# Optimization experiments

Hardware: AMD Instinct MI355X
Metric: run time of the kernel (lower is better)

The kernel has to match this reference:

```python
import jax, jax.numpy as jnp
import numpy as np

D_MODEL = 512
N_HEAD = 8
D_K = 64
EPS = 1e-5


def setup_inputs() -> dict:
    key = jax.random.key(0)
    ks = jax.random.split(key, 12)
    B, S = 4, 2048
    Q = jax.random.normal(ks[0], (B, S, D_MODEL), dtype=jnp.float32)
    K = jax.random.normal(ks[1], (B, S, D_MODEL), dtype=jnp.float32)
    V = jax.random.normal(ks[2], (B, S, D_MODEL), dtype=jnp.float32)
    # bool padding-style mask: True = masked position
    att_mask = jax.random.randint(ks[3], (B, S, S), 0, 2).astype(bool)
    s = 1.0 / np.sqrt(D_MODEL)
    # Linear weights stored as [in, out] (transpose of torch's [out, in]; same math)
    Wq = jax.random.uniform(ks[4], (D_MODEL, N_HEAD * D_K), jnp.float32, -s, s)
    bq = jax.random.uniform(ks[5], (N_HEAD * D_K,), jnp.float32, -s, s)
    Wk = jax.random.uniform(ks[6], (D_MODEL, N_HEAD * D_K), jnp.float32, -s, s)
    bk = jax.random.uniform(ks[7], (N_HEAD * D_K,), jnp.float32, -s, s)
    Wv = jax.random.uniform(ks[8], (D_MODEL, N_HEAD * D_K), jnp.float32, -s, s)
    bv = jax.random.uniform(ks[9], (N_HEAD * D_K,), jnp.float32, -s, s)
    Wo = jax.random.uniform(ks[10], (N_HEAD * D_K, D_MODEL), jnp.float32, -s, s)
    bo = jax.random.uniform(ks[11], (D_MODEL,), jnp.float32, -s, s)
    return {"Q": Q, "K": K, "V": V, "att_mask": att_mask,
            "Wq": Wq, "bq": bq, "Wk": Wk, "bk": bk,
            "Wv": Wv, "bv": bv, "Wo": Wo, "bo": bo}


def _layer_norm(x):
    # nn.LayerNorm with default weight=1, bias=0 (fresh module in forward)
    mu = jnp.mean(x, axis=-1, keepdims=True)
    var = jnp.mean(jnp.square(x - mu), axis=-1, keepdims=True)
    return (x - mu) / jnp.sqrt(var + EPS)


def reference(Q, K, V, att_mask, Wq, bq, Wk, bk, Wv, bv, Wo, bo):
    B, S, _ = Q.shape
    residual = Q
    # QKV projections -> [B, H, S, Dk]
    q = (Q @ Wq + bq).reshape(B, S, N_HEAD, D_K).transpose(0, 2, 1, 3)
    k = (K @ Wk + bk).reshape(B, S, N_HEAD, D_K).transpose(0, 2, 1, 3)
    v = (V @ Wv + bv).reshape(B, S, N_HEAD, D_K).transpose(0, 2, 1, 3)
    # scaled dot-product attention with padding mask
    score = jnp.einsum('bhqd,bhkd->bhqk', q, k) / np.sqrt(D_K)
    score = jnp.where(att_mask[:, None, :, :], jnp.float32(-1e9), score)
    attn = jax.nn.softmax(score, axis=-1)
    context = jnp.einsum('bhqk,bhkd->bhqd', attn, v)
    context = context.transpose(0, 2, 1, 3).reshape(B, S, N_HEAD * D_K)
    output = context @ Wo + bo
    out = _layer_norm(output + residual)
    return out, attn
```

## Files before the change

### kernel.cpp

```cpp
#include <hip/hip_runtime.h>
#include <hip/hip_bf16.h>
#include <cstdint>
#include <cstddef>


typedef __attribute__((ext_vector_type(8)))  short short8v;
typedef __attribute__((ext_vector_type(2)))  float f32x2;
typedef __attribute__((ext_vector_type(4)))  float f32x4;
typedef __attribute__((ext_vector_type(16))) float f32x16;

constexpr int DM = 512, S = 2048, BATCH = 4, NHEAD = 8, DK = 64;
constexpr int ROWS = BATCH * S;
constexpr int BH   = BATCH * NHEAD;
constexpr size_t OUT_ELEMS = (size_t)ROWS * DM;
constexpr size_t HFRAG = 131072;

#define ZERO16 {0.f,0.f,0.f,0.f,0.f,0.f,0.f,0.f,0.f,0.f,0.f,0.f,0.f,0.f,0.f,0.f}

__device__ __forceinline__ unsigned short f2bf(float f) {
    union { __hip_bfloat16 b; unsigned short u; } c;
    c.b = __float2bfloat16(f);
    return c.u;
}
__device__ __forceinline__ float bf2f(unsigned short u) {
    union { float f; unsigned u32; } c;
    c.u32 = (unsigned)u << 16;
    return c.f;
}

__global__ __launch_bounds__(256)
void wconv(const float* __restrict__ Wq, const float* __restrict__ Wk,
           const float* __restrict__ Wv, const float* __restrict__ Wo,
           unsigned short* __restrict__ wt)
{
    __shared__ float T[32][33];
    const float* srcs[4] = {Wq, Wk, Wv, Wo};
    const float* W = srcs[blockIdx.z];
    unsigned short* out = wt + (size_t)blockIdx.z * DM * DM;
    const int r0 = blockIdx.y * 32, c0 = blockIdx.x * 32;
    const int tid = threadIdx.x;
#pragma unroll
    for (int i = 0; i < 4; ++i) {
        int lin = tid + i * 256; int r = lin >> 5, c = lin & 31;
        T[r][c] = W[(size_t)(r0 + r) * DM + c0 + c];
    }
    __syncthreads();
#pragma unroll
    for (int i = 0; i < 4; ++i) {
        int lin = tid + i * 256; int rn = lin >> 5, ck = lin & 31;
        out[(size_t)(c0 + rn) * DM + r0 + ck] = f2bf(T[ck][rn]);
    }
}

__global__ __launch_bounds__(256)
void maskpack(const uint8_t* __restrict__ mask, unsigned* __restrict__ mb)
{
    const int t = threadIdx.x;
    const int row = blockIdx.x * 4 + (t >> 6);
    const int w = t & 63;
    const uint8_t* src = mask + (size_t)row * S + 32 * w;
    const uint4 a = *reinterpret_cast<const uint4*>(src);
    const uint4 b = *reinterpret_cast<const uint4*>(src + 16);
    const unsigned m8[8] = {a.x, a.y, a.z, a.w, b.x, b.y, b.z, b.w};
    unsigned bits = 0;
#pragma unroll
    for (int k2 = 0; k2 < 32; ++k2)
        bits |= (((m8[k2 >> 2] >> (8 * (k2 & 3))) & 0xffu) ? 1u : 0u) << k2;
    mb[(size_t)row * 64 + w] = bits;
}

__global__ __launch_bounds__(256)
void proj3_mfma(const float* __restrict__ Qin, const float* __restrict__ Kin,
                const float* __restrict__ Vin, const unsigned short* __restrict__ wt,
                const float* __restrict__ bq, const float* __restrict__ bk,
                const float* __restrict__ bv,
                unsigned short* __restrict__ qo, unsigned short* __restrict__ ko,
                unsigned short* __restrict__ vo)
{
    const int z = blockIdx.z;
    const float* X = (z == 0) ? Qin : (z == 1) ? Kin : Vin;
    const unsigned short* Wt = wt + (size_t)z * DM * DM;
    const float* bias = (z == 0) ? bq : (z == 1) ? bk : bv;
    unsigned short* Y = (z == 0) ? qo : (z == 1) ? ko : vo;
    const float scale = (z == 0) ? 0.125f : 1.0f;

    const int tid = threadIdx.x, wv = tid >> 6, l = tid & 63, lr = l & 31, lh = l >> 5;
    const int m0 = blockIdx.y * 128 + wv * 32;
    const int n0 = blockIdx.x * 64;
    const float* xp = X + (size_t)(m0 + lr) * DM + 8 * lh;
    const unsigned short* w0 = Wt + (size_t)(n0 + lr) * DM + 8 * lh;
    const unsigned short* w1 = w0 + (size_t)32 * DM;
    f32x16 acc0 = ZERO16, acc1 = ZERO16;
#pragma unroll 8
    for (int t = 0; t < 32; ++t) {
        float4 xa = *reinterpret_cast<const float4*>(xp + 16 * t);
        float4 xb = *reinterpret_cast<const float4*>(xp + 16 * t + 4);
        short8v a;
        a[0] = (short)f2bf(xa.x * scale); a[1] = (short)f2bf(xa.y * scale);
        a[2] = (short)f2bf(xa.z * scale); a[3] = (short)f2bf(xa.w * scale);
        a[4] = (short)f2bf(xb.x * scale); a[5] = (short)f2bf(xb.y * scale);
        a[6] = (short)f2bf(xb.z * scale); a[7] = (short)f2bf(xb.w * scale);
        short8v b0 = *reinterpret_cast<const short8v*>(w0 + 16 * t);
        short8v b1 = *reinterpret_cast<const short8v*>(w1 + 16 * t);
        acc0 = __builtin_amdgcn_mfma_f32_32x32x16_bf16(a, b0, acc0, 0, 0, 0);
        acc1 = __builtin_amdgcn_mfma_f32_32x32x16_bf16(a, b1, acc1, 0, 0, 0);
    }
#pragma unroll
    for (int j = 0; j < 2; ++j) {
        const f32x16 acc = j ? acc1 : acc0;
        const int n = n0 + 32 * j + lr;
        const float bvv = bias[n] * scale;
        const int h = n >> 6, d = n & 63;
#pragma unroll
        for (int r = 0; r < 16; ++r) {
            const int m = m0 + (r & 3) + 8 * (r >> 2) + 4 * lh;
            const int bb = m >> 11, s = m & (S - 1);
            const int bh = bb * NHEAD + h;
            const unsigned short val = f2bf(acc[r] + bvv);
            size_t idx;
            if (z == 0)
                idx = ((size_t)bh * S + s) * DK + d;
            else if (z == 1)
                idx = (size_t)bh * HFRAG + (size_t)(s >> 4) * 1024 + (size_t)(d >> 5) * 512
                      + (size_t)(((s & 15) + 16 * ((d & 31) >> 3)) << 3) + (d & 7);
            else
                idx = (size_t)bh * HFRAG + (size_t)(s >> 5) * 2048 + (size_t)(d >> 4) * 512
                      + (size_t)(((d & 15) + 16 * ((s & 31) >> 3)) << 3) + (s & 7);
            Y[idx] = val;
        }
    }
}

__global__ __launch_bounds__(512, 4)
void attn_fused(const unsigned short* __restrict__ q,
                const unsigned short* __restrict__ kpack,
                const unsigned short* __restrict__ vpack,
                const unsigned* __restrict__ mbits,
                float* __restrict__ attn,
                unsigned short* __restrict__ ctx)
{
    __shared__ char Pc[16 * 4096];
    __shared__ float cred[2][4][16][16];
    __shared__ float redm[8][16];
    __shared__ float reds[8][16];
    const int tid = threadIdx.x, wv = tid >> 6, l = tid & 63;
    const int lq = l & 15, lg = l >> 4;
    const int bid = blockIdx.x;
    const int bh = 4 * (bid & 7) + ((bid >> 3) & 3);
    const int q0 = (bid >> 5) * 16;
    const int b = bh >> 3, h = bh & 7;

    const unsigned short* qp = q + ((size_t)bh * S + q0 + lq) * DK + 8 * lg;
    const short8v qf0 = *reinterpret_cast<const short8v*>(qp);
    const short8v qf1 = *reinterpret_cast<const short8v*>(qp + 32);
    const unsigned short* kbase = kpack + (size_t)bh * HFRAG + (size_t)l * 8;
    f32x4 acc[16];
#pragma unroll
    for (int it = 0; it < 16; ++it) {
        const unsigned short* kc = kbase + (size_t)(16 * wv + it) * 1024;
        const short8v kf0 = *reinterpret_cast<const short8v*>(kc);
        const short8v kf1 = *reinterpret_cast<const short8v*>(kc + 512);
        f32x4 a = {0.f, 0.f, 0.f, 0.f};
        a = __builtin_amdgcn_mfma_f32_16x16x32_bf16(kf0, qf0, a, 0, 0, 0);
        a = __builtin_amdgcn_mfma_f32_16x16x32_bf16(kf1, qf1, a, 0, 0, 0);
        acc[it] = a;
    }

    const unsigned* mrow = mbits + ((size_t)b * S + q0 + lq) * 64 + 8 * wv;
    const uint4 mwa = *reinterpret_cast<const uint4*>(mrow);
    const uint4 mwb = *reinterpret_cast<const uint4*>(mrow + 4);
    const unsigned mw[8] = {mwa.x, mwa.y, mwa.z, mwa.w, mwb.x, mwb.y, mwb.z, mwb.w};
    float vmax = -3e38f;
#pragma unroll
    for (int it = 0; it < 16; ++it) {
        const unsigned word = mw[it >> 1] >> (16 * (it & 1) + 4 * lg);
#pragma unroll
        for (int r = 0; r < 4; ++r) {
            const float v = ((word >> r) & 1u) ? -1e30f : acc[it][r];
            acc[it][r] = v;
            vmax = fmaxf(vmax, v);
        }
    }
    vmax = fmaxf(vmax, __shfl_xor(vmax, 16));
    vmax = fmaxf(vmax, __shfl_xor(vmax, 32));
    if (l < 16) redm[wv][l] = vmax;
    __syncthreads();
    float rmax = redm[0][lq];
#pragma unroll
    for (int w2 = 1; w2 < 8; ++w2) rmax = fmaxf(rmax, redm[w2][lq]);

    float sum = 0.f;
#pragma unroll
    for (int it = 0; it < 16; ++it)
#pragma unroll
        for (int r = 0; r < 4; ++r) {
            const float v = __expf(acc[it][r] - rmax);
            acc[it][r] = v;
            sum += v;
        }
    sum += __shfl_xor(sum, 16);
    sum += __shfl_xor(sum, 32);
    if (l < 16) reds[wv][l] = sum;
    __syncthreads();
    float rsum = 0.f;
#pragma unroll
    for (int w2 = 0; w2 < 8; ++w2) rsum += reds[w2][lq];
    const float inv = 1.0f / rsum;

    const int swz = (lq & 7) << 4;
    char* prow = Pc + lq * 4096;
#pragma unroll
    for (int it = 0; it < 16; ++it) {
        const int n = 16 * it + 4 * lg;
        ushort4 p;
        p.x = f2bf(acc[it][0] * inv); p.y = f2bf(acc[it][1] * inv);
        p.z = f2bf(acc[it][2] * inv); p.w = f2bf(acc[it][3] * inv);
        *reinterpret_cast<ushort4*>(prow + ((2 * (256 * wv + n)) ^ swz)) = p;
    }
    __syncthreads();

    const int dt = wv & 3, kh = wv >> 2;
    const int rswz = (lq & 7) << 4;
    f32x4 pacc = {0.f, 0.f, 0.f, 0.f};
    const unsigned short* vbase = vpack + (size_t)bh * HFRAG + dt * 512 + (size_t)l * 8;
    const int wrow = 8 * kh + 2 * dt + (l >> 5);
    const int wswz = (wrow & 7) << 4;
    const int lc = l & 31;
    float* arow = attn + ((size_t)bh * S + q0 + wrow) * S;
#pragma unroll 4
    for (int s = 0; s < 32; ++s) {
        const int kk0 = kh * 1024 + 32 * s;
        const short8v a = *reinterpret_cast<const short8v*>(
            Pc + lq * 4096 + ((2 * (kk0 + 8 * lg)) ^ rswz));
        const short8v bf = *reinterpret_cast<const short8v*>(
            vbase + (size_t)(kh * 32 + s) * 2048);
        pacc = __builtin_amdgcn_mfma_f32_16x16x32_bf16(a, bf, pacc, 0, 0, 0);
        const unsigned pw = *reinterpret_cast<const unsigned*>(
            Pc + wrow * 4096 + ((128 * s + 4 * lc) ^ wswz));
        f32x2 st;
        st[0] = bf2f((unsigned short)(pw & 0xffffu));
        st[1] = bf2f((unsigned short)(pw >> 16));
        __builtin_nontemporal_store(st,
            reinterpret_cast<f32x2*>(arow + 64 * s + 2 * lc));
    }
#pragma unroll
    for (int r = 0; r < 4; ++r) cred[kh][dt][lg * 4 + r][lq] = pacc[r];
    __syncthreads();

    for (int o = tid; o < 1024; o += 512) {
        const int qq = o >> 6, dd = o & 63;
        const float val = cred[0][dd >> 4][qq][dd & 15] + cred[1][dd >> 4][qq][dd & 15];
        ctx[((size_t)(b * S + q0 + qq)) * DM + h * DK + dd] = f2bf(val);
    }
}

__global__ __launch_bounds__(512)
void out_ln(const unsigned short* __restrict__ Xc, const unsigned short* __restrict__ Wt,
            const float* __restrict__ bias, const float* __restrict__ resid,
            float* __restrict__ out)
{
    __shared__ f32x2 red[32][8];
    __shared__ f32x2 stat[32];
    const int tid = threadIdx.x, wv = tid >> 6, l = tid & 63, lr = l & 31, lh = l >> 5;
    const int m0 = blockIdx.x * 32;
    const int n0 = wv * 64;
    const unsigned short* xp = Xc + (size_t)(m0 + lr) * DM + 8 * lh;
    const unsigned short* w0 = Wt + (size_t)(n0 + lr) * DM + 8 * lh;
    const unsigned short* w1 = w0 + (size_t)32 * DM;
    f32x16 acc0 = ZERO16, acc1 = ZERO16;
#pragma unroll 8
    for (int t = 0; t < 32; ++t) {
        short8v a  = *reinterpret_cast<const short8v*>(xp + 16 * t);
        short8v b0 = *reinterpret_cast<const short8v*>(w0 + 16 * t);
        short8v b1 = *reinterpret_cast<const short8v*>(w1 + 16 * t);
        acc0 = __builtin_amdgcn_mfma_f32_32x32x16_bf16(a, b0, acc0, 0, 0, 0);
        acc1 = __builtin_amdgcn_mfma_f32_32x32x16_bf16(a, b1, acc1, 0, 0, 0);
    }
    const float bv0 = bias[n0 + lr], bv1 = bias[n0 + 32 + lr];
#pragma unroll
    for (int r = 0; r < 16; ++r) {
        const int mloc = (r & 3) + 8 * (r >> 2) + 4 * lh;
        const size_t mbase = (size_t)(m0 + mloc) * DM + n0 + lr;
        const float v0 = acc0[r] + bv0 + resid[mbase];
        const float v1 = acc1[r] + bv1 + resid[mbase + 32];
        acc0[r] = v0; acc1[r] = v1;
        float s = v0 + v1, sq = v0 * v0 + v1 * v1;
#pragma unroll
        for (int off = 16; off; off >>= 1) {
            s  += __shfl_xor(s, off);
            sq += __shfl_xor(sq, off);
        }
        if (lr == 0) { f32x2 t2; t2[0] = s; t2[1] = sq; red[mloc][wv] = t2; }
    }
    __syncthreads();
    if (tid < 32) {
        float s = 0.f, sq = 0.f;
#pragma unroll
        for (int w2 = 0; w2 < 8; ++w2) { s += red[tid][w2][0]; sq += red[tid][w2][1]; }
        const float mean = s * (1.0f / 512.0f);
        const float var = sq * (1.0f / 512.0f) - mean * mean;
        f32x2 t2; t2[0] = mean; t2[1] = rsqrtf(var + 1e-5f);
        stat[tid] = t2;
    }
    __syncthreads();
#pragma unroll
    for (int r = 0; r < 16; ++r) {
        const int mloc = (r & 3) + 8 * (r >> 2) + 4 * lh;
        const f32x2 st = stat[mloc];
        const size_t mbase = (size_t)(m0 + mloc) * DM + n0 + lr;
        out[mbase]      = (acc0[r] - st[0]) * st[1];
        out[mbase + 32] = (acc1[r] - st[0]) * st[1];
    }
}

extern "C" void kernel_launch(void* const* d_in, const int* in_sizes, int n_in,
                              void* d_out, int out_size, void* d_ws, size_t ws_size,
                              hipStream_t stream)
{
    (void)in_sizes; (void)n_in; (void)out_size; (void)ws_size;

    const float*   Qin  = (const float*)d_in[0];
    const float*   Kin  = (const float*)d_in[1];
    const float*   Vin  = (const float*)d_in[2];
    const uint8_t* mask = (const uint8_t*)d_in[3];
    const float*   Wq   = (const float*)d_in[4];
    const float*   bq   = (const float*)d_in[5];
    const float*   Wk   = (const float*)d_in[6];
    const float*   bk   = (const float*)d_in[7];
    const float*   Wv   = (const float*)d_in[8];
    const float*   bv   = (const float*)d_in[9];
    const float*   Wo   = (const float*)d_in[10];
    const float*   bo   = (const float*)d_in[11];

    float* out  = (float*)d_out;
    float* attn = out + OUT_ELEMS;

    char* w = (char*)d_ws;
    const size_t MB = 1 << 20;
    unsigned short* wt    = (unsigned short*)(w);
    unsigned short* qbf   = (unsigned short*)(w + 2  * MB);
    unsigned short* kpack = (unsigned short*)(w + 10 * MB);
    unsigned short* vpack = (unsigned short*)(w + 18 * MB);
    unsigned short* ctx   = (unsigned short*)(w + 26 * MB);
    unsigned*       mbits = (unsigned*)(w + 34 * MB);

    unsigned short* wto = wt + 3 * (size_t)DM * DM;

    wconv<<<dim3(16, 16, 4), 256, 0, stream>>>(Wq, Wk, Wv, Wo, wt);

    maskpack<<<ROWS / 4, 256, 0, stream>>>(mask, mbits);

    proj3_mfma<<<dim3(DM / 64, ROWS / 128, 3), 256, 0, stream>>>(
        Qin, Kin, Vin, wt, bq, bk, bv, qbf, kpack, vpack);

    attn_fused<<<4096, 512, 0, stream>>>(qbf, kpack, vpack, mbits, attn, ctx);

    out_ln<<<ROWS / 32, 512, 0, stream>>>(ctx, wto, bo, Qin, out);
}
```

Measured before the change: 315.3 us.

## Process two query tiles per attention block and overlap attn stores with QK

Each attention block now handles two consecutive 16-row query tiles, so the grid is halved. Half of the first tile's probability-matrix write to global memory is deferred and interleaved with the QK^T MFMA loop of the second tile, so global stores overlap compute. Stores are widened to 128-bit float4. __syncthreads is replaced with a raw LDS-wait plus s_barrier. The tradeoff is fewer blocks in flight, more register pressure from the in-loop store path, and a longer serial chain per block.

```diff
diff --git a/kernel.cpp b/kernel.cpp
--- a/kernel.cpp
+++ b/kernel.cpp
@@ -16,6 +16,9 @@
 constexpr size_t HFRAG = 131072;
 
 #define ZERO16 {0.f,0.f,0.f,0.f,0.f,0.f,0.f,0.f,0.f,0.f,0.f,0.f,0.f,0.f,0.f,0.f}
+
+#define LBAR() do { asm volatile("s_waitcnt lgkmcnt(0)" ::: "memory"); \
+                    __builtin_amdgcn_s_barrier(); } while (0)
 
 __device__ __forceinline__ unsigned short f2bf(float f) {
     union { __hip_bfloat16 b; unsigned short u; } c;
@@ -147,110 +150,135 @@
     const int lq = l & 15, lg = l >> 4;
     const int bid = blockIdx.x;
     const int bh = 4 * (bid & 7) + ((bid >> 3) & 3);
-    const int q0 = (bid >> 5) * 16;
+    const int pair = bid >> 5;
     const int b = bh >> 3, h = bh & 7;
 
-    const unsigned short* qp = q + ((size_t)bh * S + q0 + lq) * DK + 8 * lg;
-    const short8v qf0 = *reinterpret_cast<const short8v*>(qp);
-    const short8v qf1 = *reinterpret_cast<const short8v*>(qp + 32);
     const unsigned short* kbase = kpack + (size_t)bh * HFRAG + (size_t)l * 8;
-    f32x4 acc[16];
-#pragma unroll
-    for (int it = 0; it < 16; ++it) {
-        const unsigned short* kc = kbase + (size_t)(16 * wv + it) * 1024;
-        const short8v kf0 = *reinterpret_cast<const short8v*>(kc);
-        const short8v kf1 = *reinterpret_cast<const short8v*>(kc + 512);
-        f32x4 a = {0.f, 0.f, 0.f, 0.f};
-        a = __builtin_amdgcn_mfma_f32_16x16x32_bf16(kf0, qf0, a, 0, 0, 0);
-        a = __builtin_amdgcn_mfma_f32_16x16x32_bf16(kf1, qf1, a, 0, 0, 0);
-        acc[it] = a;
-    }
-
-    const unsigned* mrow = mbits + ((size_t)b * S + q0 + lq) * 64 + 8 * wv;
-    const uint4 mwa = *reinterpret_cast<const uint4*>(mrow);
-    const uint4 mwb = *reinterpret_cast<const uint4*>(mrow + 4);
-    const unsigned mw[8] = {mwa.x, mwa.y, mwa.z, mwa.w, mwb.x, mwb.y, mwb.z, mwb.w};
-    float vmax = -3e38f;
-#pragma unroll
-    for (int it = 0; it < 16; ++it) {
-        const unsigned word = mw[it >> 1] >> (16 * (it & 1) + 4 * lg);
-#pragma unroll
-        for (int r = 0; r < 4; ++r) {
-            const float v = ((word >> r) & 1u) ? -1e30f : acc[it][r];
-            acc[it][r] = v;
-            vmax = fmaxf(vmax, v);
-        }
-    }
-    vmax = fmaxf(vmax, __shfl_xor(vmax, 16));
-    vmax = fmaxf(vmax, __shfl_xor(vmax, 32));
-    if (l < 16) redm[wv][l] = vmax;
-    __syncthreads();
-    float rmax = redm[0][lq];
-#pragma unroll
-    for (int w2 = 1; w2 < 8; ++w2) rmax = fmaxf(rmax, redm[w2][lq]);
-
-    float sum = 0.f;
-#pragma unroll
-    for (int it = 0; it < 16; ++it)
-#pragma unroll
-        for (int r = 0; r < 4; ++r) {
-            const float v = __expf(acc[it][r] - rmax);
-            acc[it][r] = v;
-            sum += v;
-        }
-    sum += __shfl_xor(sum, 16);
-    sum += __shfl_xor(sum, 32);
-    if (l < 16) reds[wv][l] = sum;
-    __syncthreads();
-    float rsum = 0.f;
-#pragma unroll
-    for (int w2 = 0; w2 < 8; ++w2) rsum += reds[w2][lq];
-    const float inv = 1.0f / rsum;
-
-    const int swz = (lq & 7) << 4;
-    char* prow = Pc + lq * 4096;
-#pragma unroll
-    for (int it = 0; it < 16; ++it) {
-        const int n = 16 * it + 4 * lg;
-        ushort4 p;
-        p.x = f2bf(acc[it][0] * inv); p.y = f2bf(acc[it][1] * inv);
-        p.z = f2bf(acc[it][2] * inv); p.w = f2bf(acc[it][3] * inv);
-        *reinterpret_cast<ushort4*>(prow + ((2 * (256 * wv + n)) ^ swz)) = p;
-    }
-    __syncthreads();
-
     const int dt = wv & 3, kh = wv >> 2;
+    const unsigned short* vbase = vpack + (size_t)bh * HFRAG + dt * 512 + (size_t)l * 8;
     const int rswz = (lq & 7) << 4;
-    f32x4 pacc = {0.f, 0.f, 0.f, 0.f};
-    const unsigned short* vbase = vpack + (size_t)bh * HFRAG + dt * 512 + (size_t)l * 8;
-    const int wrow = 8 * kh + 2 * dt + (l >> 5);
-    const int wswz = (wrow & 7) << 4;
+
+    const int srow = 2 * wv + (l >> 5);
+    const int sswz = (srow & 7) << 4;
     const int lc = l & 31;
-    float* arow = attn + ((size_t)bh * S + q0 + wrow) * S;
-#pragma unroll 4
-    for (int s = 0; s < 32; ++s) {
-        const int kk0 = kh * 1024 + 32 * s;
-        const short8v a = *reinterpret_cast<const short8v*>(
-            Pc + lq * 4096 + ((2 * (kk0 + 8 * lg)) ^ rswz));
-        const short8v bf = *reinterpret_cast<const short8v*>(
-            vbase + (size_t)(kh * 32 + s) * 2048);
-        pacc = __builtin_amdgcn_mfma_f32_16x16x32_bf16(a, bf, pacc, 0, 0, 0);
-        const unsigned pw = *reinterpret_cast<const unsigned*>(
-            Pc + wrow * 4096 + ((128 * s + 4 * lc) ^ wswz));
-        f32x2 st;
-        st[0] = bf2f((unsigned short)(pw & 0xffffu));
-        st[1] = bf2f((unsigned short)(pw >> 16));
-        __builtin_nontemporal_store(st,
-            reinterpret_cast<f32x2*>(arow + 64 * s + 2 * lc));
-    }
-#pragma unroll
-    for (int r = 0; r < 4; ++r) cred[kh][dt][lg * 4 + r][lq] = pacc[r];
-    __syncthreads();
-
-    for (int o = tid; o < 1024; o += 512) {
-        const int qq = o >> 6, dd = o & 63;
-        const float val = cred[0][dd >> 4][qq][dd & 15] + cred[1][dd >> 4][qq][dd & 15];
-        ctx[((size_t)(b * S + q0 + qq)) * DM + h * DK + dd] = f2bf(val);
+
+    int q0p = -1;
+#pragma unroll
+    for (int half = 0; half < 2; ++half) {
+        const int q0 = (2 * pair + half) * 16;
+
+        const unsigned short* qp = q + ((size_t)bh * S + q0 + lq) * DK + 8 * lg;
+        const short8v qf0 = *reinterpret_cast<const short8v*>(qp);
+        const short8v qf1 = *reinterpret_cast<const short8v*>(qp + 32);
+        float* sbp = (q0p >= 0) ? attn + ((size_t)bh * S + q0p + srow) * S : nullptr;
+        f32x4 acc[16];
+#pragma unroll
+        for (int it = 0; it < 16; ++it) {
+            const unsigned short* kc = kbase + (size_t)(16 * wv + it) * 1024;
+            const short8v kf0 = *reinterpret_cast<const short8v*>(kc);
+            const short8v kf1 = *reinterpret_cast<const short8v*>(kc + 512);
+            f32x4 a = {0.f, 0.f, 0.f, 0.f};
+            a = __builtin_amdgcn_mfma_f32_16x16x32_bf16(kf0, qf0, a, 0, 0, 0);
+            a = __builtin_amdgcn_mfma_f32_16x16x32_bf16(kf1, qf1, a, 0, 0, 0);
+            acc[it] = a;
+            if (sbp && it < 8) {
+                const int jj = 8 + it;
+                const ushort4 pw = *reinterpret_cast<const ushort4*>(
+                    Pc + srow * 4096 + ((8 * lc + 256 * jj) ^ sswz));
+                f32x4 st;
+                st[0] = bf2f(pw.x); st[1] = bf2f(pw.y);
+                st[2] = bf2f(pw.z); st[3] = bf2f(pw.w);
+                __builtin_nontemporal_store(st,
+                    reinterpret_cast<f32x4*>(sbp + 4 * lc + 128 * jj));
+            }
+        }
+
+        const unsigned* mrow = mbits + ((size_t)b * S + q0 + lq) * 64 + 8 * wv;
+        const uint4 mwa = *reinterpret_cast<const uint4*>(mrow);
+        const uint4 mwb = *reinterpret_cast<const uint4*>(mrow + 4);
+        const unsigned mw[8] = {mwa.x, mwa.y, mwa.z, mwa.w,
+                                mwb.x, mwb.y, mwb.z, mwb.w};
+        float vmax = -3e38f;
+#pragma unroll
+        for (int it = 0; it < 16; ++it) {
+            const unsigned word = mw[it >> 1] >> (16 * (it & 1) + 4 * lg);
+#pragma unroll
+            for (int r = 0; r < 4; ++r) {
+                const float v = ((word >> r) & 1u) ? -1e30f : acc[it][r];
+                acc[it][r] = v;
+                vmax = fmaxf(vmax, v);
+            }
+        }
+        vmax = fmaxf(vmax, __shfl_xor(vmax, 16));
+        vmax = fmaxf(vmax, __shfl_xor(vmax, 32));
+        if (l < 16) redm[wv][l] = vmax;
+        LBAR();
+        float rmax = redm[0][lq];
+#pragma unroll
+        for (int w2 = 1; w2 < 8; ++w2) rmax = fmaxf(rmax, redm[w2][lq]);
+
+        float sum = 0.f;
+#pragma unroll
+        for (int it = 0; it < 16; ++it)
+#pragma unroll
+            for (int r = 0; r < 4; ++r) {
+                const float v = __expf(acc[it][r] - rmax);
+                acc[it][r] = v;
+                sum += v;
+            }
+        sum += __shfl_xor(sum, 16);
+        sum += __shfl_xor(sum, 32);
+        if (l < 16) reds[wv][l] = sum;
+        LBAR();
+        float rsum = 0.f;
+#pragma unroll
+        for (int w2 = 0; w2 < 8; ++w2) rsum += reds[w2][lq];
+        const float inv = 1.0f / rsum;
+
+        const int swz = (lq & 7) << 4;
+        char* prow = Pc + lq * 4096;
+#pragma unroll
+        for (int it = 0; it < 16; ++it) {
+            const int n = 16 * it + 4 * lg;
+            ushort4 p;
+            p.x = f2bf(acc[it][0] * inv); p.y = f2bf(acc[it][1] * inv);
+            p.z = f2bf(acc[it][2] * inv); p.w = f2bf(acc[it][3] * inv);
+            *reinterpret_cast<ushort4*>(prow + ((2 * (256 * wv + n)) ^ swz)) = p;
+        }
+        LBAR();
+
+        const int nstore = (half == 0) ? 8 : 16;
+        float* sbc = attn + ((size_t)bh * S + q0 + srow) * S;
+        f32x4 pacc = {0.f, 0.f, 0.f, 0.f};
+#pragma unroll 8
+        for (int s = 0; s < 32; ++s) {
+            const int kk0 = kh * 1024 + 32 * s;
+            const short8v a = *reinterpret_cast<const short8v*>(
+                Pc + lq * 4096 + ((2 * (kk0 + 8 * lg)) ^ rswz));
+            const short8v bf = *reinterpret_cast<const short8v*>(
+                vbase + (size_t)(kh * 32 + s) * 2048);
+            pacc = __builtin_amdgcn_mfma_f32_16x16x32_bf16(a, bf, pacc, 0, 0, 0);
+            if (s < nstore) {
+                const ushort4 pw = *reinterpret_cast<const ushort4*>(
+                    Pc + srow * 4096 + ((8 * lc + 256 * s) ^ sswz));
+                f32x4 st;
+                st[0] = bf2f(pw.x); st[1] = bf2f(pw.y);
+                st[2] = bf2f(pw.z); st[3] = bf2f(pw.w);
+                __builtin_nontemporal_store(st,
+                    reinterpret_cast<f32x4*>(sbc + 4 * lc + 128 * s));
+            }
+        }
+#pragma unroll
+        for (int r = 0; r < 4; ++r) cred[kh][dt][lg * 4 + r][lq] = pacc[r];
+        LBAR();
+
+        for (int o = tid; o < 1024; o += 512) {
+            const int qq = o >> 6, dd = o & 63;
+            const float val = cred[0][dd >> 4][qq][dd & 15]
+                            + cred[1][dd >> 4][qq][dd & 15];
+            ctx[((size_t)(b * S + q0 + qq)) * DM + h * DK + dd] = f2bf(val);
+        }
+        q0p = q0;
     }
 }
 
@@ -353,7 +381,7 @@
     proj3_mfma<<<dim3(DM / 64, ROWS / 128, 3), 256, 0, stream>>>(
         Qin, Kin, Vin, wt, bq, bk, bv, qbf, kpack, vpack);
 
-    attn_fused<<<4096, 512, 0, stream>>>(qbf, kpack, vpack, mbits, attn, ctx);
+    attn_fused<<<2048, 512, 0, stream>>>(qbf, kpack, vpack, mbits, attn, ctx);
 
     out_ln<<<ROWS / 32, 512, 0, stream>>>(ctx, wto, bo, Qin, out);
 }
```

Result: slower. 361.5 us (+14.7%).
